# Performance work log

Measured on AMD Instinct MI355X. Metric: run time of the kernel, lower is better.

The kernel has to match this reference:

```python
import jax, jax.numpy as jnp
import numpy as np

B, V, H = 8, 256, 128
EPS = 1e-5


def _linear(x, w, b):
    # torch nn.Linear: y = x @ W^T + b
    return jnp.einsum('...i,oi->...o', x, w) + b


def _batch_norm(x, gamma, beta):
    # BatchNorm1d with track_running_stats=False: always uses batch stats,
    # biased variance, eps=1e-5. x: [..., H]; stats over all leading dims.
    xf = x.reshape(-1, x.shape[-1])
    mean = jnp.mean(xf, axis=0)
    var = jnp.mean(jnp.square(xf - mean), axis=0)
    xn = (xf - mean) * jax.lax.rsqrt(var + EPS)
    return (xn * gamma + beta).reshape(x.shape)


def setup_inputs() -> dict:
    key = jax.random.key(0)
    ks = jax.random.split(key, 16)
    s = 1.0 / np.sqrt(H)  # torch Linear default init scale
    inp = {
        'h': jax.random.normal(ks[0], (B, V, H), jnp.float32),
        'e': jax.random.normal(ks[1], (B, V, V, H), jnp.float32),
        'graph': jax.random.randint(ks[2], (B, V, V), 0, 2) > 0,
    }
    names = ['U', 'V', 'A', 'B', 'C']
    for i, n in enumerate(names):
        inp[n + '_w'] = jax.random.uniform(ks[3 + 2 * i], (H, H), jnp.float32, -s, s)
        inp[n + '_b'] = jax.random.uniform(ks[4 + 2 * i], (H,), jnp.float32, -s, s)
    inp['gamma_h'] = jnp.ones((H,), jnp.float32)
    inp['beta_h'] = jnp.zeros((H,), jnp.float32)
    inp['gamma_e'] = jnp.ones((H,), jnp.float32)
    inp['beta_e'] = jnp.zeros((H,), jnp.float32)
    return inp


def reference(h, e, graph, U_w, U_b, V_w, V_b, A_w, A_b, B_w, B_b, C_w, C_b,
              gamma_h, beta_h, gamma_e, beta_e):
    h_in, e_in = h, e
    Uh = _linear(h, U_w, U_b)            # [B,V,H]
    Vh = _linear(h, V_w, V_b)            # [B,V,H] (source-node features)
    Ah = _linear(h, A_w, A_b)            # [B,V,H]
    Bh = _linear(h, B_w, B_b)            # [B,V,H]
    Ce = _linear(e, C_w, C_b)            # [B,V,V,H]
    # e_ij combine: Ah broadcast over dim 1, Bh over dim 2 (matches torch code)
    e_new = Ah[:, None, :, :] + Bh[:, :, None, :] + Ce   # [B,V,V,H]
    gates = jax.nn.sigmoid(e_new)
    # gated messages; graph==True marks NON-edges -> zeroed
    msg = jnp.where(graph[..., None], 0.0, gates * Vh[:, None, :, :])
    agg = jnp.sum(msg, axis=2)           # aggregation='sum' -> [B,V,H]
    h_new = Uh + agg
    h_new = _batch_norm(h_new, gamma_h, beta_h)
    e_out = _batch_norm(e_new, gamma_e, beta_e)
    h_out = h_in + jax.nn.relu(h_new)
    e_out = e_in + jax.nn.relu(e_out)
    return (h_out, e_out)
```

## Files before the change

kernel.cpp:

```cpp
#include <hip/hip_runtime.h>
#include <cstdint>
#include <cstddef>

#define HH    128
#define VV    256
#define NB    8
#define NROW  2048
#define NEROW 524288
#define PROJ  (NROW*HH)
#define EPSV  1e-5f

typedef __attribute__((ext_vector_type(8))) short short8v;
typedef __attribute__((ext_vector_type(4))) float f32x4;

__device__ inline float4 f4add(float4 a, float4 b) {
    return make_float4(a.x+b.x, a.y+b.y, a.z+b.z, a.w+b.w);
}

__device__ inline unsigned short f2bf(float x) {
    unsigned u = __float_as_uint(x);
    return (unsigned short)((u + 0x7fffu + ((u >> 16) & 1u)) >> 16);
}
__device__ inline float bf2f(unsigned short h) {
    return __uint_as_float(((unsigned)h) << 16);
}
__device__ inline void split8(float4 a, float4 b, short8v &hi, short8v &lo) {
    float v[8] = {a.x, a.y, a.z, a.w, b.x, b.y, b.z, b.w};
    #pragma unroll
    for (int i = 0; i < 8; ++i) {
        unsigned short h = f2bf(v[i]);
        hi[i] = (short)h;
        lo[i] = (short)f2bf(v[i] - bf2f(h));
    }
}

__global__ __launch_bounds__(256) void k1_proj(
    const float* __restrict__ h,
    const float* __restrict__ Uw, const float* __restrict__ Ub,
    const float* __restrict__ Vw, const float* __restrict__ Vb,
    const float* __restrict__ Aw, const float* __restrict__ Ab,
    const float* __restrict__ Bw, const float* __restrict__ Bb,
    float* __restrict__ ws)
{
    __shared__ float hs[32*136];
    const int t  = threadIdx.x;
    const int R0 = blockIdx.x * 32;
    const int m  = blockIdx.y;
    {
        const float4* src = (const float4*)(h + (size_t)R0*HH);
        #pragma unroll
        for (int ii = 0; ii < 4; ++ii) {
            int idx4 = t + 256*ii;
            int r = idx4 >> 5, c = idx4 & 31;
            *(float4*)&hs[r*136 + c*4] = src[idx4];
        }
    }
    __syncthreads();
    const int o0 = (t & 15) * 8;
    const int jg = t >> 4;
    const float* __restrict__ W  = (m==0)?Uw:(m==1)?Vw:(m==2)?Aw:Bw;
    const float* __restrict__ Bv = (m==0)?Ub:(m==1)?Vb:(m==2)?Ab:Bb;

    float acc[2][8];
    #pragma unroll
    for (int jj = 0; jj < 2; ++jj)
        #pragma unroll
        for (int d = 0; d < 8; ++d) acc[jj][d] = 0.f;
    for (int k4 = 0; k4 < 32; ++k4) {
        float4 w[8];
        #pragma unroll
        for (int d = 0; d < 8; ++d)
            w[d] = *(const float4*)(W + (size_t)(o0+d)*HH + k4*4);
        #pragma unroll
        for (int jj = 0; jj < 2; ++jj) {
            float4 ev = *(const float4*)&hs[(jg*2+jj)*136 + k4*4];
            #pragma unroll
            for (int d = 0; d < 8; ++d)
                acc[jj][d] += ev.x*w[d].x + ev.y*w[d].y
                            + ev.z*w[d].z + ev.w*w[d].w;
        }
    }
    float4 b0 = *(const float4*)(Bv + o0);
    float4 b1 = *(const float4*)(Bv + o0 + 4);
    float* outp = ws + (size_t)m * PROJ;
    #pragma unroll
    for (int jj = 0; jj < 2; ++jj) {
        int r = R0 + jg*2 + jj;
        float4 v0 = f4add(make_float4(acc[jj][0],acc[jj][1],acc[jj][2],acc[jj][3]), b0);
        float4 v1 = f4add(make_float4(acc[jj][4],acc[jj][5],acc[jj][6],acc[jj][7]), b1);
        *(float4*)(outp + (size_t)r*HH + o0)     = v0;
        *(float4*)(outp + (size_t)r*HH + o0 + 4) = v1;
    }
}

__global__ __launch_bounds__(256, 2) void k2_main(
    const float* __restrict__ e,
    const int*   __restrict__ graph,
    const float* __restrict__ Cw, const float* __restrict__ Cb,
    const float* __restrict__ ws,
    float* __restrict__ agg_out,
    float* __restrict__ esum, float* __restrict__ esumsq,
    float* __restrict__ e_new_out)
{
    __shared__ float lds[2][64 * 132];
    const int t  = threadIdx.x;
    const int l  = t & 63;
    const int wv = t >> 6;
    const int bi = blockIdx.x;
    const int b  = bi >> 8;
    const int ob = wv * 32;
    const int lr = l & 15;
    const int lg = l >> 4;

    const float* __restrict__ Vh = ws + (size_t)PROJ;
    const float* __restrict__ Ah = ws + 2*(size_t)PROJ;
    const float* __restrict__ Bh = ws + 3*(size_t)PROJ;

    const int o0 = ob + lr, o1 = o0 + 16;
    const float bh0 = Bh[(size_t)bi*HH + o0];
    const float bh1 = Bh[(size_t)bi*HH + o1];
    const float cb0 = Cb[o0], cb1 = Cb[o1];

    short8v Whi[2][4], Wlo[2][4];
    #pragma unroll
    for (int n = 0; n < 2; ++n)
        #pragma unroll
        for (int kk = 0; kk < 4; ++kk) {
            const float* wp = Cw + (size_t)(ob + n*16 + lr)*HH + kk*32 + lg*8;
            split8(*(const float4*)wp, *(const float4*)(wp + 4),
                   Whi[n][kk], Wlo[n][kk]);
        }

    const float4* esrc = (const float4*)(e + (size_t)bi * VV * HH);
    float4 pf[8];
    #pragma unroll
    for (int ii = 0; ii < 8; ++ii) pf[ii] = esrc[t + 256*ii];
    #pragma unroll
    for (int ii = 0; ii < 8; ++ii) {
        int idx4 = t + 256*ii, r = idx4 >> 5, c = idx4 & 31;
        *(float4*)&lds[0][r*132 + c*4] = pf[ii];
    }
    __syncthreads();

    float se0 = 0.f, se1 = 0.f, sq0 = 0.f, sq1 = 0.f, agg0 = 0.f, agg1 = 0.f;

    #pragma unroll 1
    for (int p = 0; p < 4; ++p) {
        if (p < 3) {
            const float4* s2 = esrc + (size_t)(p + 1) * 64 * 32;
            #pragma unroll
            for (int ii = 0; ii < 8; ++ii) pf[ii] = s2[t + 256*ii];
        }

        const float* buf = lds[p & 1];
        f32x4 acc[4][2] = {};

        #pragma unroll
        for (int kk = 0; kk < 4; ++kk) {
            short8v Ahi[4], Alo[4];
            #pragma unroll
            for (int m = 0; m < 4; ++m) {
                const float* ap = buf + (m*16 + lr)*132 + kk*32 + lg*8;
                split8(*(const float4*)ap, *(const float4*)(ap + 4),
                       Ahi[m], Alo[m]);
            }
            #pragma unroll
            for (int m = 0; m < 4; ++m)
                #pragma unroll
                for (int n = 0; n < 2; ++n) {
                    acc[m][n] = __builtin_amdgcn_mfma_f32_16x16x32_bf16(
                                    Ahi[m], Whi[n][kk], acc[m][n], 0, 0, 0);
                    acc[m][n] = __builtin_amdgcn_mfma_f32_16x16x32_bf16(
                                    Ahi[m], Wlo[n][kk], acc[m][n], 0, 0, 0);
                    acc[m][n] = __builtin_amdgcn_mfma_f32_16x16x32_bf16(
                                    Alo[m], Whi[n][kk], acc[m][n], 0, 0, 0);
                }
        }

        #pragma unroll
        for (int m = 0; m < 4; ++m)
            #pragma unroll
            for (int r = 0; r < 4; ++r) {
                const int j = p*64 + m*16 + lg*4 + r;
                const float* AhR = Ah + (size_t)(b*VV + j)*HH;
                const float* VhR = Vh + (size_t)(b*VV + j)*HH;
                const float gm = graph[(size_t)bi*VV + j] ? 0.f : 1.f;
                float* eo = e_new_out + ((size_t)bi*VV + j)*HH;
                float v0 = acc[m][0][r] + cb0 + bh0 + AhR[o0];
                float v1 = acc[m][1][r] + cb1 + bh1 + AhR[o1];
                eo[o0] = v0; eo[o1] = v1;
                se0 += v0; sq0 += v0*v0;
                se1 += v1; sq1 += v1*v1;
                agg0 += gm * VhR[o0] / (1.f + __expf(-v0));
                agg1 += gm * VhR[o1] / (1.f + __expf(-v1));
            }

        if (p < 3) {
            float* dst = lds[(p + 1) & 1];
            #pragma unroll
            for (int ii = 0; ii < 8; ++ii) {
                int idx4 = t + 256*ii, r = idx4 >> 5, c = idx4 & 31;
                *(float4*)&dst[r*132 + c*4] = pf[ii];
            }
            __syncthreads();
        }
    }

    se0 += __shfl_xor(se0, 16); se0 += __shfl_xor(se0, 32);
    sq0 += __shfl_xor(sq0, 16); sq0 += __shfl_xor(sq0, 32);
    se1 += __shfl_xor(se1, 16); se1 += __shfl_xor(se1, 32);
    sq1 += __shfl_xor(sq1, 16); sq1 += __shfl_xor(sq1, 32);
    agg0 += __shfl_xor(agg0, 16); agg0 += __shfl_xor(agg0, 32);
    agg1 += __shfl_xor(agg1, 16); agg1 += __shfl_xor(agg1, 32);
    if (l < 16) {
        const int oA = ob + l, oB = oA + 16;
        atomicAdd(&esum[oA],   se0);  atomicAdd(&esumsq[oA], sq0);
        atomicAdd(&esum[oB],   se1);  atomicAdd(&esumsq[oB], sq1);
        agg_out[(size_t)bi*HH + oA] = agg0;
        agg_out[(size_t)bi*HH + oB] = agg1;
    }
}

__global__ __launch_bounds__(256) void k3a_hnew(
    const float* __restrict__ Uh, const float* __restrict__ agg,
    float* __restrict__ hnew, float* __restrict__ hsum, float* __restrict__ hsumsq)
{
    __shared__ float red[512];
    const int t = threadIdx.x;
    const int o = t & 127;
    const int g = t >> 7;
    const int R0 = blockIdx.x * 16;
    float s = 0.f, s2 = 0.f;
    #pragma unroll
    for (int rr = 0; rr < 8; ++rr) {
        size_t idx = (size_t)(R0 + g*8 + rr)*HH + o;
        float v = Uh[idx] + agg[idx];
        hnew[idx] = v;
        s += v; s2 += v*v;
    }
    red[t] = s; red[256 + t] = s2;
    __syncthreads();
    if (t < 128) {
        atomicAdd(&hsum[o],   red[t]     + red[t + 128]);
        atomicAdd(&hsumsq[o], red[256+t] + red[256 + t + 128]);
    }
}

__global__ void k3b_coef(const float* __restrict__ st, float* __restrict__ coef,
    const float* __restrict__ gh, const float* __restrict__ bh,
    const float* __restrict__ ge, const float* __restrict__ be)
{
    int o = threadIdx.x;
    float es = st[o], eq = st[128+o], hs = st[256+o], hq = st[384+o];
    float me = es * (1.f/(float)NEROW);
    float ve = eq * (1.f/(float)NEROW) - me*me;
    float ae = ge[o] * rsqrtf(ve + EPSV);
    float ce = be[o] - me*ae;
    float mh = hs * (1.f/(float)NROW);
    float vh = hq * (1.f/(float)NROW) - mh*mh;
    float ah = gh[o] * rsqrtf(vh + EPSV);
    float ch = bh[o] - mh*ah;
    coef[o] = ah; coef[128+o] = ch; coef[256+o] = ae; coef[384+o] = ce;
}

__global__ __launch_bounds__(256) void k3c_hout(
    const float* __restrict__ h_in, const float* __restrict__ hnew,
    const float* __restrict__ coef, float* __restrict__ out_h)
{
    int idx = blockIdx.x*256 + threadIdx.x;
    int o4 = (idx & 31) * 4;
    float4 a = *(const float4*)(coef + o4);
    float4 c = *(const float4*)(coef + 128 + o4);
    float4 v = ((const float4*)hnew)[idx];
    float4 x = ((const float4*)h_in)[idx];
    float4 r;
    r.x = x.x + fmaxf(fmaf(a.x, v.x, c.x), 0.f);
    r.y = x.y + fmaxf(fmaf(a.y, v.y, c.y), 0.f);
    r.z = x.z + fmaxf(fmaf(a.z, v.z, c.z), 0.f);
    r.w = x.w + fmaxf(fmaf(a.w, v.w, c.w), 0.f);
    ((float4*)out_h)[idx] = r;
}

__global__ __launch_bounds__(256) void k4_eout(
    const float* __restrict__ e_in, const float* __restrict__ coef,
    float* __restrict__ e_io)
{
    const size_t total4 = (size_t)NEROW * HH / 4;
    size_t idx = (size_t)blockIdx.x * 256 + threadIdx.x;
    const size_t stride = (size_t)gridDim.x * 256;
    const int o4 = ((int)(idx & 31)) * 4;
    const float4 a = *(const float4*)(coef + 256 + o4);
    const float4 c = *(const float4*)(coef + 384 + o4);
    const float4* ein4 = (const float4*)e_in;
    float4* eio4 = (float4*)e_io;
    for (; idx < total4; idx += stride) {
        float4 v = eio4[idx];
        float4 x = ein4[idx];
        float4 r;
        r.x = x.x + fmaxf(fmaf(a.x, v.x, c.x), 0.f);
        r.y = x.y + fmaxf(fmaf(a.y, v.y, c.y), 0.f);
        r.z = x.z + fmaxf(fmaf(a.z, v.z, c.z), 0.f);
        r.w = x.w + fmaxf(fmaf(a.w, v.w, c.w), 0.f);
        eio4[idx] = r;
    }
}

extern "C" void kernel_launch(void* const* d_in, const int* in_sizes, int n_in,
                              void* d_out, int out_size, void* d_ws, size_t ws_size,
                              hipStream_t stream)
{
    (void)in_sizes; (void)n_in; (void)out_size; (void)ws_size;
    const float* h     = (const float*)d_in[0];
    const float* e     = (const float*)d_in[1];
    const int*   graph = (const int*)  d_in[2];
    const float* Uw = (const float*)d_in[3];
    const float* Ub = (const float*)d_in[4];
    const float* Vw = (const float*)d_in[5];
    const float* Vb = (const float*)d_in[6];
    const float* Aw = (const float*)d_in[7];
    const float* Ab = (const float*)d_in[8];
    const float* Bw = (const float*)d_in[9];
    const float* Bb = (const float*)d_in[10];
    const float* Cw = (const float*)d_in[11];
    const float* Cb = (const float*)d_in[12];
    const float* gamma_h = (const float*)d_in[13];
    const float* beta_h  = (const float*)d_in[14];
    const float* gamma_e = (const float*)d_in[15];
    const float* beta_e  = (const float*)d_in[16];

    float* out_h = (float*)d_out;
    float* out_e = out_h + (size_t)NROW * HH;

    float* ws    = (float*)d_ws;
    float* Uh    = ws;
    float* aggp  = ws + 4*(size_t)PROJ;
    float* hnew  = ws + 5*(size_t)PROJ;
    float* stats = ws + 6*(size_t)PROJ;
    float* coef  = stats + 512;

    hipMemsetAsync(stats, 0, 512*sizeof(float), stream);
    k1_proj<<<dim3(64, 4), 256, 0, stream>>>(h, Uw,Ub, Vw,Vb, Aw,Ab, Bw,Bb, ws);
    k2_main<<<2048, 256, 0, stream>>>(e, graph, Cw, Cb, ws, aggp,
                                      stats, stats+128, out_e);
    k3a_hnew<<<128, 256, 0, stream>>>(Uh, aggp, hnew, stats+256, stats+384);
    k3b_coef<<<1, 128, 0, stream>>>(stats, coef, gamma_h, beta_h, gamma_e, beta_e);
    k3c_hout<<<256, 256, 0, stream>>>(h, hnew, coef, out_h);
    k4_eout<<<8192, 256, 0, stream>>>(e, coef, out_e);
}
```

Baseline: 770.3 us.

## Store e_new in fp16 and pre-split bf16 hi/lo tiles in LDS

```diff
diff --git a/kernel.cpp b/kernel.cpp
--- a/kernel.cpp
+++ b/kernel.cpp
@@ -11,7 +11,9 @@
 #define EPSV  1e-5f
 
 typedef __attribute__((ext_vector_type(8))) short short8v;
+typedef __attribute__((ext_vector_type(4))) short short4v;
 typedef __attribute__((ext_vector_type(4))) float f32x4;
+typedef __attribute__((ext_vector_type(4))) _Float16 f16x4;
 
 __device__ inline float4 f4add(float4 a, float4 b) {
     return make_float4(a.x+b.x, a.y+b.y, a.z+b.z, a.w+b.w);
@@ -23,6 +25,15 @@
 }
 __device__ inline float bf2f(unsigned short h) {
     return __uint_as_float(((unsigned)h) << 16);
+}
+__device__ inline void split4(float4 v, short4v &hi, short4v &lo) {
+    float a[4] = {v.x, v.y, v.z, v.w};
+    #pragma unroll
+    for (int i = 0; i < 4; ++i) {
+        unsigned short h = f2bf(a[i]);
+        hi[i] = (short)h;
+        lo[i] = (short)f2bf(a[i] - bf2f(h));
+    }
 }
 __device__ inline void split8(float4 a, float4 b, short8v &hi, short8v &lo) {
     float v[8] = {a.x, a.y, a.z, a.w, b.x, b.y, b.z, b.w};
@@ -93,131 +104,174 @@
     }
 }
 
-__global__ __launch_bounds__(256, 2) void k2_main(
+template<int HALF>
+__global__ __launch_bounds__(256, 3) void k2_main(
     const float* __restrict__ e,
     const int*   __restrict__ graph,
     const float* __restrict__ Cw, const float* __restrict__ Cb,
     const float* __restrict__ ws,
     float* __restrict__ agg_out,
     float* __restrict__ esum, float* __restrict__ esumsq,
-    float* __restrict__ e_new_out)
-{
-    __shared__ float lds[2][64 * 132];
-    const int t  = threadIdx.x;
-    const int l  = t & 63;
-    const int wv = t >> 6;
-    const int bi = blockIdx.x;
-    const int b  = bi >> 8;
-    const int ob = wv * 32;
-    const int lr = l & 15;
-    const int lg = l >> 4;
+    float* __restrict__ e_new_f, _Float16* __restrict__ e_new_h)
+{
+    __shared__ short sh[2][2][32*136];
+    const int t   = threadIdx.x;
+    const int l   = t & 63;
+    const int wv  = t >> 6;
+    const int bi  = blockIdx.x;
+    const int b   = bi >> 8;
+    const int ob  = wv * 32;
+    const int lr  = l & 15;
+    const int lg  = l >> 4;
+    const int lg4 = lg * 4, lg8 = lg * 8;
 
     const float* __restrict__ Vh = ws + (size_t)PROJ;
     const float* __restrict__ Ah = ws + 2*(size_t)PROJ;
     const float* __restrict__ Bh = ws + 3*(size_t)PROJ;
 
-    const int o0 = ob + lr, o1 = o0 + 16;
-    const float bh0 = Bh[(size_t)bi*HH + o0];
-    const float bh1 = Bh[(size_t)bi*HH + o1];
-    const float cb0 = Cb[o0], cb1 = Cb[o1];
+    f32x4 bc4[2];
+    #pragma unroll
+    for (int nt = 0; nt < 2; ++nt) {
+        const int oo = ob + nt*16 + lg4;
+        f32x4 bh = *(const f32x4*)(Bh + (size_t)bi*HH + oo);
+        f32x4 cb = *(const f32x4*)(Cb + oo);
+        bc4[nt] = bh + cb;
+    }
 
     short8v Whi[2][4], Wlo[2][4];
     #pragma unroll
-    for (int n = 0; n < 2; ++n)
+    for (int nt = 0; nt < 2; ++nt)
         #pragma unroll
         for (int kk = 0; kk < 4; ++kk) {
-            const float* wp = Cw + (size_t)(ob + n*16 + lr)*HH + kk*32 + lg*8;
+            const float* wp = Cw + (size_t)(ob + nt*16 + lr)*HH + kk*32 + lg8;
             split8(*(const float4*)wp, *(const float4*)(wp + 4),
-                   Whi[n][kk], Wlo[n][kk]);
+                   Whi[nt][kk], Wlo[nt][kk]);
         }
 
     const float4* esrc = (const float4*)(e + (size_t)bi * VV * HH);
-    float4 pf[8];
-    #pragma unroll
-    for (int ii = 0; ii < 8; ++ii) pf[ii] = esrc[t + 256*ii];
-    #pragma unroll
-    for (int ii = 0; ii < 8; ++ii) {
-        int idx4 = t + 256*ii, r = idx4 >> 5, c = idx4 & 31;
-        *(float4*)&lds[0][r*132 + c*4] = pf[ii];
+
+    float4 pf[4];
+    #pragma unroll
+    for (int q = 0; q < 4; ++q) pf[q] = esrc[t + 256*q];
+    #pragma unroll
+    for (int q = 0; q < 4; ++q) {
+        int idx4 = t + 256*q, r = idx4 >> 5, c4 = idx4 & 31;
+        short4v hv, lv; split4(pf[q], hv, lv);
+        *(short4v*)&sh[0][0][r*136 + c4*4] = hv;
+        *(short4v*)&sh[0][1][r*136 + c4*4] = lv;
     }
     __syncthreads();
 
-    float se0 = 0.f, se1 = 0.f, sq0 = 0.f, sq1 = 0.f, agg0 = 0.f, agg1 = 0.f;
+    f32x4 se4[2], sq4[2], agg4[2];
+    #pragma unroll
+    for (int nt = 0; nt < 2; ++nt) {
+        se4[nt] = (f32x4)0.f; sq4[nt] = (f32x4)0.f; agg4[nt] = (f32x4)0.f;
+    }
 
     #pragma unroll 1
-    for (int p = 0; p < 4; ++p) {
-        if (p < 3) {
-            const float4* s2 = esrc + (size_t)(p + 1) * 64 * 32;
-            #pragma unroll
-            for (int ii = 0; ii < 8; ++ii) pf[ii] = s2[t + 256*ii];
-        }
-
-        const float* buf = lds[p & 1];
-        f32x4 acc[4][2] = {};
+    for (int p = 0; p < 8; ++p) {
+        if (p < 7) {
+            const float4* s2 = esrc + (size_t)(p + 1) * 1024;
+            #pragma unroll
+            for (int q = 0; q < 4; ++q) pf[q] = s2[t + 256*q];
+        }
+
+        const short* hiT = &sh[p & 1][0][0];
+        const short* loT = &sh[p & 1][1][0];
+        f32x4 acc[2][2];
+        #pragma unroll
+        for (int mt = 0; mt < 2; ++mt)
+            #pragma unroll
+            for (int nt = 0; nt < 2; ++nt) acc[mt][nt] = (f32x4)0.f;
 
         #pragma unroll
         for (int kk = 0; kk < 4; ++kk) {
-            short8v Ahi[4], Alo[4];
-            #pragma unroll
-            for (int m = 0; m < 4; ++m) {
-                const float* ap = buf + (m*16 + lr)*132 + kk*32 + lg*8;
-                split8(*(const float4*)ap, *(const float4*)(ap + 4),
-                       Ahi[m], Alo[m]);
+            short8v Eh[2], El[2];
+            #pragma unroll
+            for (int mt = 0; mt < 2; ++mt) {
+                const int off = (mt*16 + lr)*136 + kk*32 + lg8;
+                Eh[mt] = *(const short8v*)&hiT[off];
+                El[mt] = *(const short8v*)&loT[off];
             }
             #pragma unroll
-            for (int m = 0; m < 4; ++m)
+            for (int mt = 0; mt < 2; ++mt)
                 #pragma unroll
-                for (int n = 0; n < 2; ++n) {
-                    acc[m][n] = __builtin_amdgcn_mfma_f32_16x16x32_bf16(
-                                    Ahi[m], Whi[n][kk], acc[m][n], 0, 0, 0);
-                    acc[m][n] = __builtin_amdgcn_mfma_f32_16x16x32_bf16(
-                                    Ahi[m], Wlo[n][kk], acc[m][n], 0, 0, 0);
-                    acc[m][n] = __builtin_amdgcn_mfma_f32_16x16x32_bf16(
-                                    Alo[m], Whi[n][kk], acc[m][n], 0, 0, 0);
+                for (int nt = 0; nt < 2; ++nt) {
+                    acc[mt][nt] = __builtin_amdgcn_mfma_f32_16x16x32_bf16(
+                                      Whi[nt][kk], Eh[mt], acc[mt][nt], 0, 0, 0);
+                    acc[mt][nt] = __builtin_amdgcn_mfma_f32_16x16x32_bf16(
+                                      Wlo[nt][kk], Eh[mt], acc[mt][nt], 0, 0, 0);
+                    acc[mt][nt] = __builtin_amdgcn_mfma_f32_16x16x32_bf16(
+                                      Whi[nt][kk], El[mt], acc[mt][nt], 0, 0, 0);
                 }
         }
 
         #pragma unroll
-        for (int m = 0; m < 4; ++m)
-            #pragma unroll
-            for (int r = 0; r < 4; ++r) {
-                const int j = p*64 + m*16 + lg*4 + r;
-                const float* AhR = Ah + (size_t)(b*VV + j)*HH;
-                const float* VhR = Vh + (size_t)(b*VV + j)*HH;
-                const float gm = graph[(size_t)bi*VV + j] ? 0.f : 1.f;
-                float* eo = e_new_out + ((size_t)bi*VV + j)*HH;
-                float v0 = acc[m][0][r] + cb0 + bh0 + AhR[o0];
-                float v1 = acc[m][1][r] + cb1 + bh1 + AhR[o1];
-                eo[o0] = v0; eo[o1] = v1;
-                se0 += v0; sq0 += v0*v0;
-                se1 += v1; sq1 += v1*v1;
-                agg0 += gm * VhR[o0] / (1.f + __expf(-v0));
-                agg1 += gm * VhR[o1] / (1.f + __expf(-v1));
+        for (int mt = 0; mt < 2; ++mt) {
+            const int j = p*32 + mt*16 + lr;
+            const size_t rowA = (size_t)(b*VV + j) * HH;
+            const size_t rowE = ((size_t)bi*VV + j) * HH;
+            const float gm = graph[(size_t)bi*VV + j] ? 0.f : 1.f;
+            #pragma unroll
+            for (int nt = 0; nt < 2; ++nt) {
+                const int oo = ob + nt*16 + lg4;
+                f32x4 A4 = *(const f32x4*)(Ah + rowA + oo);
+                f32x4 V4 = *(const f32x4*)(Vh + rowA + oo);
+                f32x4 en = acc[mt][nt] + bc4[nt] + A4;
+                if (HALF) {
+                    f16x4 hv;
+                    #pragma unroll
+                    for (int c = 0; c < 4; ++c) hv[c] = (_Float16)en[c];
+                    *(f16x4*)&e_new_h[rowE + oo] = hv;
+                } else {
+                    *(f32x4*)&e_new_f[rowE + oo] = en;
+                }
+                se4[nt] += en;
+                sq4[nt] += en * en;
+                f32x4 sg;
+                #pragma unroll
+                for (int c = 0; c < 4; ++c)
+                    sg[c] = 1.f / (1.f + __expf(-en[c]));
+                agg4[nt] += (gm * V4) * sg;
             }
-
-        if (p < 3) {
-            float* dst = lds[(p + 1) & 1];
-            #pragma unroll
-            for (int ii = 0; ii < 8; ++ii) {
-                int idx4 = t + 256*ii, r = idx4 >> 5, c = idx4 & 31;
-                *(float4*)&dst[r*132 + c*4] = pf[ii];
+        }
+
+        if (p < 7) {
+            short* dh = &sh[(p+1) & 1][0][0];
+            short* dl = &sh[(p+1) & 1][1][0];
+            #pragma unroll
+            for (int q = 0; q < 4; ++q) {
+                int idx4 = t + 256*q, r = idx4 >> 5, c4 = idx4 & 31;
+                short4v hv, lv; split4(pf[q], hv, lv);
+                *(short4v*)&dh[r*136 + c4*4] = hv;
+                *(short4v*)&dl[r*136 + c4*4] = lv;
             }
             __syncthreads();
         }
     }
 
-    se0 += __shfl_xor(se0, 16); se0 += __shfl_xor(se0, 32);
-    sq0 += __shfl_xor(sq0, 16); sq0 += __shfl_xor(sq0, 32);
-    se1 += __shfl_xor(se1, 16); se1 += __shfl_xor(se1, 32);
-    sq1 += __shfl_xor(sq1, 16); sq1 += __shfl_xor(sq1, 32);
-    agg0 += __shfl_xor(agg0, 16); agg0 += __shfl_xor(agg0, 32);
-    agg1 += __shfl_xor(agg1, 16); agg1 += __shfl_xor(agg1, 32);
-    if (l < 16) {
-        const int oA = ob + l, oB = oA + 16;
-        atomicAdd(&esum[oA],   se0);  atomicAdd(&esumsq[oA], sq0);
-        atomicAdd(&esum[oB],   se1);  atomicAdd(&esumsq[oB], sq1);
-        agg_out[(size_t)bi*HH + oA] = agg0;
-        agg_out[(size_t)bi*HH + oB] = agg1;
+    #pragma unroll
+    for (int m = 1; m < 16; m <<= 1) {
+        #pragma unroll
+        for (int nt = 0; nt < 2; ++nt)
+            #pragma unroll
+            for (int c = 0; c < 4; ++c) {
+                se4[nt][c]  += __shfl_xor(se4[nt][c],  m);
+                sq4[nt][c]  += __shfl_xor(sq4[nt][c],  m);
+                agg4[nt][c] += __shfl_xor(agg4[nt][c], m);
+            }
+    }
+    if (lr == 0) {
+        #pragma unroll
+        for (int nt = 0; nt < 2; ++nt) {
+            const int oo = ob + nt*16 + lg4;
+            *(f32x4*)&agg_out[(size_t)bi*HH + oo] = agg4[nt];
+            #pragma unroll
+            for (int c = 0; c < 4; ++c) {
+                atomicAdd(&esum[oo + c],   se4[nt][c]);
+                atomicAdd(&esumsq[oo + c], sq4[nt][c]);
+            }
+        }
     }
 }
 
@@ -281,9 +335,10 @@
     ((float4*)out_h)[idx] = r;
 }
 
+template<int HALF>
 __global__ __launch_bounds__(256) void k4_eout(
     const float* __restrict__ e_in, const float* __restrict__ coef,
-    float* __restrict__ e_io)
+    const void* __restrict__ enew, float* __restrict__ e_out)
 {
     const size_t total4 = (size_t)NEROW * HH / 4;
     size_t idx = (size_t)blockIdx.x * 256 + threadIdx.x;
@@ -292,16 +347,21 @@
     const float4 a = *(const float4*)(coef + 256 + o4);
     const float4 c = *(const float4*)(coef + 384 + o4);
     const float4* ein4 = (const float4*)e_in;
-    float4* eio4 = (float4*)e_io;
     for (; idx < total4; idx += stride) {
-        float4 v = eio4[idx];
+        float4 v;
+        if (HALF) {
+            f16x4 hv = ((const f16x4*)enew)[idx];
+            v = make_float4((float)hv[0], (float)hv[1], (float)hv[2], (float)hv[3]);
+        } else {
+            v = ((const float4*)enew)[idx];
+        }
         float4 x = ein4[idx];
         float4 r;
         r.x = x.x + fmaxf(fmaf(a.x, v.x, c.x), 0.f);
         r.y = x.y + fmaxf(fmaf(a.y, v.y, c.y), 0.f);
         r.z = x.z + fmaxf(fmaf(a.z, v.z, c.z), 0.f);
         r.w = x.w + fmaxf(fmaf(a.w, v.w, c.w), 0.f);
-        eio4[idx] = r;
+        ((float4*)e_out)[idx] = r;
     }
 }
 
@@ -309,7 +369,7 @@
                               void* d_out, int out_size, void* d_ws, size_t ws_size,
                               hipStream_t stream)
 {
-    (void)in_sizes; (void)n_in; (void)out_size; (void)ws_size;
+    (void)in_sizes; (void)n_in; (void)out_size;
     const float* h     = (const float*)d_in[0];
     const float* e     = (const float*)d_in[1];
     const int*   graph = (const int*)  d_in[2];
@@ -338,12 +398,26 @@
     float* stats = ws + 6*(size_t)PROJ;
     float* coef  = stats + 512;
 
+    size_t base = ((size_t)(6*PROJ + 1024) * 4 + 255) & ~(size_t)255;
+    size_t need = base + (size_t)NEROW * HH * 2;
+    bool use_half = (ws_size >= need);
+    _Float16* enh = (_Float16*)((char*)d_ws + base);
+
     hipMemsetAsync(stats, 0, 512*sizeof(float), stream);
     k1_proj<<<dim3(64, 4), 256, 0, stream>>>(h, Uw,Ub, Vw,Vb, Aw,Ab, Bw,Bb, ws);
-    k2_main<<<2048, 256, 0, stream>>>(e, graph, Cw, Cb, ws, aggp,
-                                      stats, stats+128, out_e);
+    if (use_half) {
+        k2_main<1><<<2048, 256, 0, stream>>>(e, graph, Cw, Cb, ws, aggp,
+                                             stats, stats+128, out_e, enh);
+    } else {
+        k2_main<0><<<2048, 256, 0, stream>>>(e, graph, Cw, Cb, ws, aggp,
+                                             stats, stats+128, out_e, enh);
+    }
     k3a_hnew<<<128, 256, 0, stream>>>(Uh, aggp, hnew, stats+256, stats+384);
     k3b_coef<<<1, 128, 0, stream>>>(stats, coef, gamma_h, beta_h, gamma_e, beta_e);
     k3c_hout<<<256, 256, 0, stream>>>(h, hnew, coef, out_h);
-    k4_eout<<<8192, 256, 0, stream>>>(e, coef, out_e);
-}
+    if (use_half) {
+        k4_eout<1><<<8192, 256, 0, stream>>>(e, coef, enh, out_e);
+    } else {
+        k4_eout<0><<<8192, 256, 0, stream>>>(e, coef, out_e, out_e);
+    }
+}
```

Measured after the change: 786.7 us. 1.02x slower.
